# Performance work log

Measured on AMD Instinct MI355X. Metric: run time of the kernel, lower is better.

Reference implementation:

```python
import jax, jax.numpy as jnp
import numpy as np

D = 1024
H = 16
HD = D // H
SCALE = HD ** -0.5
EPS = 1e-5

def _ln(x, g, b):
    m = jnp.mean(x, axis=-1, keepdims=True)
    v = jnp.mean((x - m) ** 2, axis=-1, keepdims=True)
    return (x - m) / jnp.sqrt(v + EPS) * g + b

def setup_inputs() -> dict:
    key = jax.random.key(0)
    ks = jax.random.split(key, 16)
    B, Lq, Lk = 8, 1024, 1024
    s = 0.02
    inp = {
        "q": jax.random.normal(ks[0], (B, Lq, D), jnp.float32),
        "kv": jax.random.normal(ks[1], (B, Lk, D), jnp.float32),
        "kv_mask": jax.random.randint(ks[2], (B, Lk), 0, 2).astype(bool),
        "Wq": jax.random.normal(ks[3], (D, D), jnp.float32) * s,
        "bq": jnp.zeros((D,), jnp.float32),
        "Wk": jax.random.normal(ks[4], (D, D), jnp.float32) * s,
        "bk": jnp.zeros((D,), jnp.float32),
        "Wv": jax.random.normal(ks[5], (D, D), jnp.float32) * s,
        "bv": jnp.zeros((D,), jnp.float32),
        "Wo": jax.random.normal(ks[6], (D, D), jnp.float32) * s,
        "bo": jnp.zeros((D,), jnp.float32),
        "ln1_g": jnp.ones((D,), jnp.float32),
        "ln1_b": jnp.zeros((D,), jnp.float32),
        "W1": jax.random.normal(ks[7], (D, 4 * D), jnp.float32) * s,
        "b1": jnp.zeros((4 * D,), jnp.float32),
        "W2": jax.random.normal(ks[8], (4 * D, D), jnp.float32) * s,
        "b2": jnp.zeros((D,), jnp.float32),
        "ln2_g": jnp.ones((D,), jnp.float32),
        "ln2_b": jnp.zeros((D,), jnp.float32),
    }
    return inp

def reference(q, kv, kv_mask, Wq, bq, Wk, bk, Wv, bv, Wo, bo, ln1_g, ln1_b, W1, b1, W2, b2, ln2_g, ln2_b):
    B, Lq, _ = q.shape
    Lk = kv.shape[1]
    # projections -> [B, H, L, HD]
    qp = (q @ Wq + bq).reshape(B, Lq, H, HD).transpose(0, 2, 1, 3)
    kp = (kv @ Wk + bk).reshape(B, Lk, H, HD).transpose(0, 2, 1, 3)
    vp = (kv @ Wv + bv).reshape(B, Lk, H, HD).transpose(0, 2, 1, 3)
    scores = jnp.einsum('bhqd,bhkd->bhqk', qp, kp) * SCALE
    # mask: True = pad; if a row is all-pad, un-mask the last key position
    all_pad = jnp.all(kv_mask, axis=1)  # [B]
    mask = kv_mask.at[:, -1].set(jnp.where(all_pad, False, kv_mask[:, -1]))
    scores = jnp.where(mask[:, None, None, :], jnp.float32(-10000.0), scores)
    attn = jax.nn.softmax(scores, axis=-1)  # dropout is identity at eval
    out = jnp.einsum('bhqk,bhkd->bhqd', attn, vp)
    out = out.transpose(0, 2, 1, 3).reshape(B, Lq, D)
    out = out @ Wo + bo
    x = _ln(q + out, ln1_g, ln1_b)
    x2 = jax.nn.relu(x @ W1 + b1) @ W2 + b2
    return _ln(x + x2, ln2_g, ln2_b)
```

## Files before the change

### kernel.cpp

```cpp
#include <hip/hip_runtime.h>

typedef __bf16 bf16_t;
typedef bf16_t bf16x8 __attribute__((ext_vector_type(8)));
typedef bf16_t bf16x4 __attribute__((ext_vector_type(4)));
typedef float f32x4 __attribute__((ext_vector_type(4)));
typedef unsigned int u32;

typedef __attribute__((address_space(1))) unsigned as1_u32;
typedef __attribute__((address_space(3))) unsigned as3_u32;

#define LOG2E 1.4426950408889634f
#define QSCALE (0.125f * LOG2E)
#define MASK2 (-10000.0f * LOG2E)

__device__ __forceinline__ void gload16(const void* g, void* l) {
  __builtin_amdgcn_global_load_lds((as1_u32*)(void*)g, (as3_u32*)l, 16, 0, 0);
}

__global__ void cvt_qkv(const float* __restrict__ q, const float* __restrict__ kv,
                        bf16_t* __restrict__ qb, bf16_t* __restrict__ kvb) {
  long i = ((long)blockIdx.x * 256 + threadIdx.x) * 8;
  const float* src; bf16_t* dst;
  if (i < 8388608) { src = q + i; dst = qb + i; }
  else { src = kv + (i - 8388608); dst = kvb + (i - 8388608); }
  const float4 a = *(const float4*)src;
  const float4 b = *(const float4*)(src + 4);
  bf16x8 o;
  o[0] = (bf16_t)a.x; o[1] = (bf16_t)a.y; o[2] = (bf16_t)a.z; o[3] = (bf16_t)a.w;
  o[4] = (bf16_t)b.x; o[5] = (bf16_t)b.y; o[6] = (bf16_t)b.z; o[7] = (bf16_t)b.w;
  *(bf16x8*)dst = o;
}

__global__ void prep_mask(const unsigned char* __restrict__ mraw,
                          float* __restrict__ maskf) {
  __shared__ int sred[256];
  const int t = threadIdx.x, b = blockIdx.x;
  int f = 0;
  for (int i = t; i < 2048; i += 256) {
    u32 v = ((const u32*)mraw)[i];
    if (v & 0xFFFFFF00u) f = 1;
  }
  sred[t] = f; __syncthreads();
  for (int s = 128; s; s >>= 1) { if (t < s) sred[t] |= sred[t + s]; __syncthreads(); }
  const int isByte = sred[0];
  __syncthreads();

  int vals[4]; int allpad = 1;
#pragma unroll
  for (int i = 0; i < 4; i++) {
    int k = t * 4 + i;
    int mv = isByte ? (int)mraw[b * 1024 + k] : ((const int*)mraw)[b * 1024 + k];
    vals[i] = (mv != 0);
    allpad &= vals[i];
  }
  sred[t] = allpad; __syncthreads();
  for (int s = 128; s; s >>= 1) { if (t < s) sred[t] &= sred[t + s]; __syncthreads(); }
  const int ap = sred[0];
#pragma unroll
  for (int i = 0; i < 4; i++) {
    int k = t * 4 + i;
    int m = vals[i];
    if (ap && k == 1023) m = 0;
    maskf[b * 1024 + k] = m ? MASK2 : 0.0f;
  }
}

struct TP { const float* s; bf16_t* d; int K; int N; };
struct TP6 { TP t[6]; };
__global__ void transpose_all(TP6 args) {
  __shared__ float tile[64][65];
  int bid = blockIdx.x, z, tx, ty;
  if (bid < 1024)      { z = bid >> 8;  int r = bid & 255;  tx = r & 15; ty = r >> 4; }
  else if (bid < 2048) { z = 4;         int r = bid - 1024; tx = r & 63; ty = r >> 6; }
  else                 { z = 5;         int r = bid - 2048; tx = r & 15; ty = r >> 4; }
  const TP a = args.t[z];
  const int t = threadIdx.x;
  const int n0 = tx * 64, k0 = ty * 64;
#pragma unroll
  for (int i = 0; i < 16; i++) {
    int e = i * 256 + t; int r = e >> 6, c = e & 63;
    tile[r][c] = a.s[(size_t)(k0 + r) * a.N + n0 + c];
  }
  __syncthreads();
#pragma unroll
  for (int i = 0; i < 16; i++) {
    int e = i * 256 + t; int r = e >> 6, c = e & 63;
    a.d[(size_t)(n0 + r) * a.K + k0 + c] = (bf16_t)tile[c][r];
  }
}

__global__ __launch_bounds__(256)
void gemm_bt(const bf16_t* __restrict__ A, const bf16_t* __restrict__ BT,
             const float* __restrict__ bias, bf16_t* __restrict__ C,
             int M, int N, int K, int relu, int bias_mode, float scale) {
  __shared__ __align__(16) bf16_t As[128 * 32];
  __shared__ __align__(16) bf16_t Bs[128 * 32];
  const int tid = threadIdx.x;
  const int wave = tid >> 6, lane = tid & 63;
  const int quad = lane >> 4, l15 = lane & 15;
  const int gx = gridDim.x;
  const int nwg = gx * gridDim.y;
  int lin = blockIdx.y * gx + blockIdx.x;
  lin = (lin & 7) * (nwg >> 3) + (lin >> 3);
  const long bm = (long)(lin / gx) * 128, bn = (long)(lin % gx) * 128;
  const int wm = (wave >> 1) * 64, wn = (wave & 1) * 64;

  f32x4 acc[4][4];
#pragma unroll
  for (int i = 0; i < 4; i++)
#pragma unroll
    for (int j = 0; j < 4; j++) acc[i][j] = (f32x4){0.f, 0.f, 0.f, 0.f};

  const bf16_t* ag = A + (bm + wave * 32 + (lane >> 2)) * (long)K + (lane & 3) * 8;
  const bf16_t* bg = BT + (bn + wave * 32 + (lane >> 2)) * (long)K + (lane & 3) * 8;
  bf16_t* as_dst = &As[wave * 1024];
  bf16_t* bs_dst = &Bs[wave * 1024];

  for (int k0 = 0; k0 < K; k0 += 32) {
    gload16(ag + k0, as_dst);
    gload16(ag + k0 + (long)16 * K, as_dst + 512);
    gload16(bg + k0, bs_dst);
    gload16(bg + k0 + (long)16 * K, bs_dst + 512);
    __syncthreads();

    bf16x8 af[4], bf[4];
#pragma unroll
    for (int i = 0; i < 4; i++)
      af[i] = *(const bf16x8*)&As[(wm + i * 16 + l15) * 32 + quad * 8];
#pragma unroll
    for (int i = 0; i < 4; i++)
      bf[i] = *(const bf16x8*)&Bs[(wn + i * 16 + l15) * 32 + quad * 8];
#pragma unroll
    for (int mi = 0; mi < 4; mi++)
#pragma unroll
      for (int ni = 0; ni < 4; ni++)
        acc[mi][ni] = __builtin_amdgcn_mfma_f32_16x16x32_bf16(af[mi], bf[ni], acc[mi][ni], 0, 0, 0);
    __syncthreads();
  }

#pragma unroll
  for (int mi = 0; mi < 4; mi++) {
#pragma unroll
    for (int ni = 0; ni < 4; ni++) {
      const long col = bn + wn + ni * 16 + l15;
      const float bc = bias_mode ? 0.f : bias[col];
#pragma unroll
      for (int r = 0; r < 4; r++) {
        const long row = bm + wm + mi * 16 + quad * 4 + r;
        const float bb = bias_mode ? bias[row] : bc;
        float v = (acc[mi][ni][r] + bb) * scale;
        if (relu) v = v > 0.f ? v : 0.f;
        C[row * N + col] = (bf16_t)v;
      }
    }
  }
}

__global__ __launch_bounds__(256, 4)
void attn(const bf16_t* __restrict__ Q, const bf16_t* __restrict__ Kp,
          const bf16_t* __restrict__ Vt, const float* __restrict__ maskf,
          bf16_t* __restrict__ AO) {
  __shared__ __align__(16) bf16_t Qs[64 * 64];
  __shared__ __align__(16) bf16_t Ks[64 * 64];
  __shared__ __align__(16) bf16_t Vts[64 * 64];
  __shared__ __align__(16) bf16_t Ps[4][16 * 64];
  __shared__ __align__(16) float msk[64];

  const int tid = threadIdx.x;
  const int wave = tid >> 6, lane = tid & 63;
  const int quad = lane >> 4, l15 = lane & 15;
  int lin = (blockIdx.z * 16 + blockIdx.y) * 16 + blockIdx.x;
  lin = (lin & 7) * 256 + (lin >> 3);
  const int q0 = (lin & 15) * 64;
  const int h = (lin >> 4) & 15;
  const int b = lin >> 8;

  const long base_q = ((long)b * 1024 + q0) * 1024 + h * 64;
  const long base_k = (long)b * 1024 * 1024 + h * 64;
  const long base_v = (long)h * 64 * 8192 + b * 1024;

  const int r0 = tid >> 3;
  const int c0 = ((tid & 7) ^ (r0 & 7)) * 8;
  const int r1 = (256 + tid) >> 3;
  const int c1 = (((256 + tid) & 7) ^ (r1 & 7)) * 8;
  const int wd0 = wave * 64 * 8;
  const int wd1 = (256 + wave * 64) * 8;

  const bf16_t* qg0 = Q + base_q + (long)r0 * 1024 + c0;
  const bf16_t* qg1 = Q + base_q + (long)r1 * 1024 + c1;
  const bf16_t* kg0 = Kp + base_k + (long)r0 * 1024 + c0;
  const bf16_t* kg1 = Kp + base_k + (long)r1 * 1024 + c1;
  const bf16_t* vg0 = Vt + base_v + (long)r0 * 8192 + c0;
  const bf16_t* vg1 = Vt + base_v + (long)r1 * 8192 + c1;
  const float* mrow = maskf + b * 1024;

  gload16(qg0, &Qs[wd0]);
  gload16(qg1, &Qs[wd1]);

  int offKV[4][2], offP[2], pwOff[4];
#pragma unroll
  for (int nt = 0; nt < 4; nt++)
#pragma unroll
    for (int ks = 0; ks < 2; ks++)
      offKV[nt][ks] = (nt * 16 + l15) * 64 + (((ks * 4 + quad) ^ (l15 & 7)) * 8);
#pragma unroll
  for (int ks = 0; ks < 2; ks++)
    offP[ks] = l15 * 64 + (((ks * 4 + quad) ^ (l15 & 7)) * 8);
#pragma unroll
  for (int nt = 0; nt < 4; nt++)
    pwOff[nt] = l15 * 64 + (((nt * 2 + (quad >> 1)) ^ (l15 & 7)) * 8) + (quad & 1) * 4;

  __syncthreads();

  bf16x8 aq[2];
#pragma unroll
  for (int ks = 0; ks < 2; ks++) {
    const int row = wave * 16 + l15;
    aq[ks] = *(const bf16x8*)&Qs[row * 64 + (((ks * 4 + quad) ^ (row & 7)) * 8)];
  }

  float m_i = -1e30f, l_i = 0.f;
  f32x4 o[4];
#pragma unroll
  for (int nt = 0; nt < 4; nt++) o[nt] = (f32x4){0.f, 0.f, 0.f, 0.f};

  bf16_t* Pw = &Ps[wave][0];

  for (int kt = 0; kt < 16; kt++) {
    const int k0 = kt * 64;
    __syncthreads();
    gload16(kg0 + (long)k0 * 1024, &Ks[wd0]);
    gload16(kg1 + (long)k0 * 1024, &Ks[wd1]);
    gload16(vg0 + k0, &Vts[wd0]);
    gload16(vg1 + k0, &Vts[wd1]);
    if (tid < 64) msk[tid] = mrow[k0 + tid];
    __syncthreads();

    f32x4 mv[4];
#pragma unroll
    for (int nt = 0; nt < 4; nt++)
      mv[nt] = *(const f32x4*)&msk[nt * 16 + quad * 4];

    f32x4 sc[4];
#pragma unroll
    for (int nt = 0; nt < 4; nt++) {
      f32x4 s = mv[nt];
#pragma unroll
      for (int ks = 0; ks < 2; ks++) {
        bf16x8 bk = *(const bf16x8*)&Ks[offKV[nt][ks]];
        s = __builtin_amdgcn_mfma_f32_16x16x32_bf16(bk, aq[ks], s, 0, 0, 0);
      }
      sc[nt] = s;
    }

    float mx = -1e30f;
#pragma unroll
    for (int nt = 0; nt < 4; nt++)
#pragma unroll
      for (int r = 0; r < 4; r++) mx = fmaxf(mx, sc[nt][r]);
    mx = fmaxf(mx, __shfl_xor(mx, 16));
    mx = fmaxf(mx, __shfl_xor(mx, 32));
    const float mnew = fmaxf(m_i, mx);
    const float alpha = exp2f(m_i - mnew);
    m_i = mnew;
    float ps = 0.f;
#pragma unroll
    for (int nt = 0; nt < 4; nt++)
#pragma unroll
      for (int r = 0; r < 4; r++) {
        const float p = exp2f(sc[nt][r] - mnew);
        sc[nt][r] = p;
        ps += p;
      }
    ps += __shfl_xor(ps, 16);
    ps += __shfl_xor(ps, 32);
    l_i = l_i * alpha + ps;

    float a4[4];
#pragma unroll
    for (int r = 0; r < 4; r++)
      a4[r] = __shfl(alpha, (quad << 4) | (quad * 4 + r));
#pragma unroll
    for (int nt = 0; nt < 4; nt++)
#pragma unroll
      for (int r = 0; r < 4; r++) o[nt][r] *= a4[r];

#pragma unroll
    for (int nt = 0; nt < 4; nt++) {
      bf16x4 pv;
#pragma unroll
      for (int r = 0; r < 4; r++) pv[r] = (bf16_t)sc[nt][r];
      *(bf16x4*)&Pw[pwOff[nt]] = pv;
    }

#pragma unroll
    for (int ks = 0; ks < 2; ks++) {
      bf16x8 ap = *(const bf16x8*)&Pw[offP[ks]];
#pragma unroll
      for (int nt = 0; nt < 4; nt++) {
        bf16x8 bv = *(const bf16x8*)&Vts[offKV[nt][ks]];
        o[nt] = __builtin_amdgcn_mfma_f32_16x16x32_bf16(ap, bv, o[nt], 0, 0, 0);
      }
    }
  }

  float linv[4];
#pragma unroll
  for (int r = 0; r < 4; r++)
    linv[r] = 1.0f / __shfl(l_i, (quad << 4) | (quad * 4 + r));
#pragma unroll
  for (int r = 0; r < 4; r++) {
    const int row = q0 + wave * 16 + quad * 4 + r;
#pragma unroll
    for (int nt = 0; nt < 4; nt++) {
      const int col = h * 64 + nt * 16 + l15;
      AO[((long)b * 1024 + row) * 1024 + col] = (bf16_t)(o[nt][r] * linv[r]);
    }
  }
}

__global__ __launch_bounds__(256)
void ln_res1(const float* __restrict__ xa, const bf16_t* __restrict__ xb,
             const float* __restrict__ g, const float* __restrict__ bt,
             bf16_t* __restrict__ out) {
  __shared__ float sw[8];
  const int t = threadIdx.x, w = t >> 6;
  const long row = blockIdx.x;
  const float4 a = *(const float4*)(xa + row * 1024 + t * 4);
  const bf16x4 bq = *(const bf16x4*)(xb + row * 1024 + t * 4);
  float v[4] = {a.x + (float)bq[0], a.y + (float)bq[1],
                a.z + (float)bq[2], a.w + (float)bq[3]};
  float s = v[0] + v[1] + v[2] + v[3];
  float s2 = v[0]*v[0] + v[1]*v[1] + v[2]*v[2] + v[3]*v[3];
#pragma unroll
  for (int off = 1; off < 64; off <<= 1) {
    s += __shfl_xor(s, off); s2 += __shfl_xor(s2, off);
  }
  if ((t & 63) == 0) { sw[w] = s; sw[4 + w] = s2; }
  __syncthreads();
  s = sw[0] + sw[1] + sw[2] + sw[3];
  s2 = sw[4] + sw[5] + sw[6] + sw[7];
  const float mean = s * (1.f / 1024.f);
  const float var = s2 * (1.f / 1024.f) - mean * mean;
  const float rstd = rsqrtf(var + 1e-5f);
  bf16x4 o;
#pragma unroll
  for (int i = 0; i < 4; i++) {
    const int c = t * 4 + i;
    o[i] = (bf16_t)((v[i] - mean) * rstd * g[c] + bt[c]);
  }
  *(bf16x4*)(out + row * 1024 + t * 4) = o;
}

__global__ __launch_bounds__(256)
void ln_res2(const bf16_t* __restrict__ xa, const bf16_t* __restrict__ xb,
             const float* __restrict__ g, const float* __restrict__ bt,
             float* __restrict__ out) {
  __shared__ float sw[8];
  const int t = threadIdx.x, w = t >> 6;
  const long row = blockIdx.x;
  const bf16x4 aq = *(const bf16x4*)(xa + row * 1024 + t * 4);
  const bf16x4 bq = *(const bf16x4*)(xb + row * 1024 + t * 4);
  float v[4];
#pragma unroll
  for (int i = 0; i < 4; i++) v[i] = (float)aq[i] + (float)bq[i];
  float s = v[0] + v[1] + v[2] + v[3];
  float s2 = v[0]*v[0] + v[1]*v[1] + v[2]*v[2] + v[3]*v[3];
#pragma unroll
  for (int off = 1; off < 64; off <<= 1) {
    s += __shfl_xor(s, off); s2 += __shfl_xor(s2, off);
  }
  if ((t & 63) == 0) { sw[w] = s; sw[4 + w] = s2; }
  __syncthreads();
  s = sw[0] + sw[1] + sw[2] + sw[3];
  s2 = sw[4] + sw[5] + sw[6] + sw[7];
  const float mean = s * (1.f / 1024.f);
  const float var = s2 * (1.f / 1024.f) - mean * mean;
  const float rstd = rsqrtf(var + 1e-5f);
  float4 o;
  o.x = (v[0] - mean) * rstd * g[t*4+0] + bt[t*4+0];
  o.y = (v[1] - mean) * rstd * g[t*4+1] + bt[t*4+1];
  o.z = (v[2] - mean) * rstd * g[t*4+2] + bt[t*4+2];
  o.w = (v[3] - mean) * rstd * g[t*4+3] + bt[t*4+3];
  *(float4*)(out + row * 1024 + t * 4) = o;
}

extern "C" void kernel_launch(void* const* d_in, const int* in_sizes, int n_in,
                              void* d_out, int out_size, void* d_ws, size_t ws_size,
                              hipStream_t stream) {
  (void)in_sizes; (void)n_in; (void)out_size; (void)ws_size;
  const float* q   = (const float*)d_in[0];
  const float* kv  = (const float*)d_in[1];
  const unsigned char* mraw = (const unsigned char*)d_in[2];
  const float* Wq = (const float*)d_in[3];
  const float* bq = (const float*)d_in[4];
  const float* Wk = (const float*)d_in[5];
  const float* bk = (const float*)d_in[6];
  const float* Wv = (const float*)d_in[7];
  const float* bv = (const float*)d_in[8];
  const float* Wo = (const float*)d_in[9];
  const float* bo = (const float*)d_in[10];
  const float* g1 = (const float*)d_in[11];
  const float* be1 = (const float*)d_in[12];
  const float* W1 = (const float*)d_in[13];
  const float* b1 = (const float*)d_in[14];
  const float* W2 = (const float*)d_in[15];
  const float* b2 = (const float*)d_in[16];
  const float* g2 = (const float*)d_in[17];
  const float* be2 = (const float*)d_in[18];
  float* out = (float*)d_out;

  char* ws = (char*)d_ws;
  size_t off = 0;
  auto alloc = [&](size_t bytes) -> char* {
    char* p = ws + off; off += (bytes + 255) & ~(size_t)255; return p;
  };
  const size_t MB16 = (size_t)8192 * 1024 * 2;
  float*  maskf = (float*)alloc(8192 * 4);
  bf16_t* WqT = (bf16_t*)alloc((size_t)1024 * 1024 * 2);
  bf16_t* WkT = (bf16_t*)alloc((size_t)1024 * 1024 * 2);
  bf16_t* WvT = (bf16_t*)alloc((size_t)1024 * 1024 * 2);
  bf16_t* WoT = (bf16_t*)alloc((size_t)1024 * 1024 * 2);
  bf16_t* W1T = (bf16_t*)alloc((size_t)1024 * 4096 * 2);
  bf16_t* W2T = (bf16_t*)alloc((size_t)4096 * 1024 * 2);
  bf16_t* Qp = (bf16_t*)alloc(MB16);
  bf16_t* Kp = (bf16_t*)alloc(MB16);
  bf16_t* VT = (bf16_t*)alloc(MB16);
  bf16_t* AO = (bf16_t*)alloc(MB16);
  bf16_t* X1 = (bf16_t*)alloc(MB16);
  bf16_t* TL = (bf16_t*)alloc(MB16);
  bf16_t* qb  = X1;
  bf16_t* kvb = TL;
  bf16_t* HF  = Qp;
  bf16_t* OP  = Kp;
  bf16_t* F2  = WqT;

  cvt_qkv<<<8192, 256, 0, stream>>>(q, kv, qb, kvb);
  prep_mask<<<8, 256, 0, stream>>>(mraw, maskf);
  TP6 tp = {{ {Wq, WqT, 1024, 1024}, {Wk, WkT, 1024, 1024},
              {Wv, WvT, 1024, 1024}, {Wo, WoT, 1024, 1024},
              {W1, W1T, 1024, 4096}, {W2, W2T, 4096, 1024} }};
  transpose_all<<<3072, 256, 0, stream>>>(tp);

  const dim3 gproj(8, 64);
  gemm_bt<<<gproj, 256, 0, stream>>>(qb,  WqT, bq, Qp, 8192, 1024, 1024, 0, 0, QSCALE);
  gemm_bt<<<gproj, 256, 0, stream>>>(kvb, WkT, bk, Kp, 8192, 1024, 1024, 0, 0, 1.f);
  gemm_bt<<<dim3(64, 8), 256, 0, stream>>>(WvT, kvb, bv, VT, 1024, 8192, 1024, 0, 1, 1.f);

  attn<<<dim3(16, 16, 8), 256, 0, stream>>>(Qp, Kp, VT, maskf, AO);

  gemm_bt<<<gproj, 256, 0, stream>>>(AO, WoT, bo, OP, 8192, 1024, 1024, 0, 0, 1.f);
  ln_res1<<<8192, 256, 0, stream>>>(q, OP, g1, be1, X1);

  gemm_bt<<<dim3(32, 64), 256, 0, stream>>>(X1, W1T, b1, HF, 8192, 4096, 1024, 1, 0, 1.f);
  gemm_bt<<<dim3(8, 64), 256, 0, stream>>>(HF, W2T, b2, F2, 8192, 1024, 4096, 0, 0, 1.f);
  ln_res2<<<8192, 256, 0, stream>>>(X1, F2, g2, be2, out);
}
```

Before: 640.6 us.

## Double-buffer GEMM LDS tiles with BK=64, XOR swizzle and prefetch

Rewrites the bf16 GEMM main loop to use a K-tile of 64 with two LDS stages. The next tile's global-to-LDS loads are issued before computing on the current one, with a partial vmcnt wait. LDS reads use an XOR swizzle to avoid bank conflicts, and MFMA blocks are wrapped in setprio. The aim is to hide global load latency and reduce barrier and bank-conflict stalls in all projection and FFN GEMMs. The cost is double the LDS footprint (64KB per block), which may limit occupancy, plus dependence on correct hand-written waitcnt counts.

```diff
diff --git a/kernel.cpp b/kernel.cpp
--- a/kernel.cpp
+++ b/kernel.cpp
@@ -89,12 +89,22 @@
   }
 }
 
-__global__ __launch_bounds__(256)
+template<int BM, int BN, int NT>
+__global__ __launch_bounds__(NT, 2)
 void gemm_bt(const bf16_t* __restrict__ A, const bf16_t* __restrict__ BT,
              const float* __restrict__ bias, bf16_t* __restrict__ C,
              int M, int N, int K, int relu, int bias_mode, float scale) {
-  __shared__ __align__(16) bf16_t As[128 * 32];
-  __shared__ __align__(16) bf16_t Bs[128 * 32];
+  constexpr int WAVES = NT / 64;
+  constexpr int WNC = (BN == 256) ? 4 : 2;
+  constexpr int WMC = WAVES / WNC;
+  constexpr int M_REP = BM / (WMC * 16);
+  constexpr int N_REP = BN / (WNC * 16);
+  constexpr int JA = BM * 8 / NT;
+  constexpr int JB = BN * 8 / NT;
+
+  __shared__ __align__(16) bf16_t As[2][BM * 64];
+  __shared__ __align__(16) bf16_t Bs[2][BN * 64];
+
   const int tid = threadIdx.x;
   const int wave = tid >> 6, lane = tid & 63;
   const int quad = lane >> 4, l15 = lane & 15;
@@ -102,46 +112,88 @@
   const int nwg = gx * gridDim.y;
   int lin = blockIdx.y * gx + blockIdx.x;
   lin = (lin & 7) * (nwg >> 3) + (lin >> 3);
-  const long bm = (long)(lin / gx) * 128, bn = (long)(lin % gx) * 128;
-  const int wm = (wave >> 1) * 64, wn = (wave & 1) * 64;
-
-  f32x4 acc[4][4];
-#pragma unroll
-  for (int i = 0; i < 4; i++)
-#pragma unroll
-    for (int j = 0; j < 4; j++) acc[i][j] = (f32x4){0.f, 0.f, 0.f, 0.f};
-
-  const bf16_t* ag = A + (bm + wave * 32 + (lane >> 2)) * (long)K + (lane & 3) * 8;
-  const bf16_t* bg = BT + (bn + wave * 32 + (lane >> 2)) * (long)K + (lane & 3) * 8;
-  bf16_t* as_dst = &As[wave * 1024];
-  bf16_t* bs_dst = &Bs[wave * 1024];
-
-  for (int k0 = 0; k0 < K; k0 += 32) {
-    gload16(ag + k0, as_dst);
-    gload16(ag + k0 + (long)16 * K, as_dst + 512);
-    gload16(bg + k0, bs_dst);
-    gload16(bg + k0 + (long)16 * K, bs_dst + 512);
-    __syncthreads();
-
-    bf16x8 af[4], bf[4];
-#pragma unroll
-    for (int i = 0; i < 4; i++)
-      af[i] = *(const bf16x8*)&As[(wm + i * 16 + l15) * 32 + quad * 8];
-#pragma unroll
-    for (int i = 0; i < 4; i++)
-      bf[i] = *(const bf16x8*)&Bs[(wn + i * 16 + l15) * 32 + quad * 8];
-#pragma unroll
-    for (int mi = 0; mi < 4; mi++)
-#pragma unroll
-      for (int ni = 0; ni < 4; ni++)
-        acc[mi][ni] = __builtin_amdgcn_mfma_f32_16x16x32_bf16(af[mi], bf[ni], acc[mi][ni], 0, 0, 0);
-    __syncthreads();
-  }
-
-#pragma unroll
-  for (int mi = 0; mi < 4; mi++) {
-#pragma unroll
-    for (int ni = 0; ni < 4; ni++) {
+  const long bm = (long)(lin / gx) * BM, bn = (long)(lin % gx) * BN;
+  const int wm = (wave / WNC) * (M_REP * 16), wn = (wave % WNC) * (N_REP * 16);
+
+  const bf16_t* agp[JA];
+  const bf16_t* bgp[JB];
+#pragma unroll
+  for (int j = 0; j < JA; j++) {
+    int e = j * NT + tid, r = e >> 3, c = (e & 7) ^ (r & 7);
+    agp[j] = A + (bm + r) * (long)K + c * 8;
+  }
+#pragma unroll
+  for (int j = 0; j < JB; j++) {
+    int e = j * NT + tid, r = e >> 3, c = (e & 7) ^ (r & 7);
+    bgp[j] = BT + (bn + r) * (long)K + c * 8;
+  }
+
+  int aoff[M_REP][2], boff[N_REP][2];
+#pragma unroll
+  for (int mi = 0; mi < M_REP; mi++)
+#pragma unroll
+    for (int ks = 0; ks < 2; ks++) {
+      int row = wm + mi * 16 + l15;
+      aoff[mi][ks] = row * 64 + (((ks * 4 + quad) ^ (row & 7)) * 8);
+    }
+#pragma unroll
+  for (int ni = 0; ni < N_REP; ni++)
+#pragma unroll
+    for (int ks = 0; ks < 2; ks++) {
+      int row = wn + ni * 16 + l15;
+      boff[ni][ks] = row * 64 + (((ks * 4 + quad) ^ (row & 7)) * 8);
+    }
+
+  f32x4 acc[M_REP][N_REP];
+#pragma unroll
+  for (int i = 0; i < M_REP; i++)
+#pragma unroll
+    for (int j = 0; j < N_REP; j++) acc[i][j] = (f32x4){0.f, 0.f, 0.f, 0.f};
+
+  auto stage = [&](int kt, int s) {
+#pragma unroll
+    for (int j = 0; j < JA; j++)
+      gload16(agp[j] + (long)kt * 64, &As[s][(j * NT + wave * 64) * 8]);
+#pragma unroll
+    for (int j = 0; j < JB; j++)
+      gload16(bgp[j] + (long)kt * 64, &Bs[s][(j * NT + wave * 64) * 8]);
+  };
+
+  const int T = K >> 6;
+  stage(0, 0);
+  for (int t = 0; t < T; t++) {
+    const int s = t & 1;
+    if (t + 1 < T) {
+      stage(t + 1, s ^ 1);
+      asm volatile("s_waitcnt vmcnt(8)" ::: "memory");
+    } else {
+      asm volatile("s_waitcnt vmcnt(0)" ::: "memory");
+    }
+    __builtin_amdgcn_s_barrier();
+
+#pragma unroll
+    for (int ks = 0; ks < 2; ks++) {
+      bf16x8 af[M_REP], bf[N_REP];
+#pragma unroll
+      for (int mi = 0; mi < M_REP; mi++) af[mi] = *(const bf16x8*)&As[s][aoff[mi][ks]];
+#pragma unroll
+      for (int ni = 0; ni < N_REP; ni++) bf[ni] = *(const bf16x8*)&Bs[s][boff[ni][ks]];
+      __builtin_amdgcn_s_setprio(1);
+#pragma unroll
+      for (int mi = 0; mi < M_REP; mi++)
+#pragma unroll
+        for (int ni = 0; ni < N_REP; ni++)
+          acc[mi][ni] = __builtin_amdgcn_mfma_f32_16x16x32_bf16(af[mi], bf[ni], acc[mi][ni], 0, 0, 0);
+      __builtin_amdgcn_s_setprio(0);
+    }
+    asm volatile("s_waitcnt lgkmcnt(0)" ::: "memory");
+    __builtin_amdgcn_s_barrier();
+  }
+
+#pragma unroll
+  for (int mi = 0; mi < M_REP; mi++) {
+#pragma unroll
+    for (int ni = 0; ni < N_REP; ni++) {
       const long col = bn + wn + ni * 16 + l15;
       const float bc = bias_mode ? 0.f : bias[col];
 #pragma unroll
@@ -443,16 +495,16 @@
   transpose_all<<<3072, 256, 0, stream>>>(tp);
 
   const dim3 gproj(8, 64);
-  gemm_bt<<<gproj, 256, 0, stream>>>(qb,  WqT, bq, Qp, 8192, 1024, 1024, 0, 0, QSCALE);
-  gemm_bt<<<gproj, 256, 0, stream>>>(kvb, WkT, bk, Kp, 8192, 1024, 1024, 0, 0, 1.f);
-  gemm_bt<<<dim3(64, 8), 256, 0, stream>>>(WvT, kvb, bv, VT, 1024, 8192, 1024, 0, 1, 1.f);
+  gemm_bt<128,128,256><<<gproj, 256, 0, stream>>>(qb,  WqT, bq, Qp, 8192, 1024, 1024, 0, 0, QSCALE);
+  gemm_bt<128,128,256><<<gproj, 256, 0, stream>>>(kvb, WkT, bk, Kp, 8192, 1024, 1024, 0, 0, 1.f);
+  gemm_bt<128,128,256><<<dim3(64, 8), 256, 0, stream>>>(WvT, kvb, bv, VT, 1024, 8192, 1024, 0, 1, 1.f);
 
   attn<<<dim3(16, 16, 8), 256, 0, stream>>>(Qp, Kp, VT, maskf, AO);
 
-  gemm_bt<<<gproj, 256, 0, stream>>>(AO, WoT, bo, OP, 8192, 1024, 1024, 0, 0, 1.f);
+  gemm_bt<128,128,256><<<gproj, 256, 0, stream>>>(AO, WoT, bo, OP, 8192, 1024, 1024, 0, 0, 1.f);
   ln_res1<<<8192, 256, 0, stream>>>(q, OP, g1, be1, X1);
 
-  gemm_bt<<<dim3(32, 64), 256, 0, stream>>>(X1, W1T, b1, HF, 8192, 4096, 1024, 1, 0, 1.f);
-  gemm_bt<<<dim3(8, 64), 256, 0, stream>>>(HF, W2T, b2, F2, 8192, 1024, 4096, 0, 0, 1.f);
+  gemm_bt<128,128,256><<<dim3(32, 64), 256, 0, stream>>>(X1, W1T, b1, HF, 8192, 4096, 1024, 1, 0, 1.f);
+  gemm_bt<128,128,256><<<gproj, 256, 0, stream>>>(HF, W2T, b2, F2, 8192, 1024, 4096, 0, 0, 1.f);
   ln_res2<<<8192, 256, 0, stream>>>(X1, F2, g2, be2, out);
 }
```

Result: faster. 585.8 us (-8.6%).
